# Kernel optimization log

Hardware: AMD Instinct MI355X
Metric: run time of the kernel (lower is better)

The kernel has to match this reference:

```python
import jax, jax.numpy as jnp
import numpy as np
from jax import lax

D_MODEL = 768
D_STATE = 16
D_CONV = 4
EXPAND = 1
D_INNER = D_MODEL * EXPAND  # 768
BATCH, SEQ = 8, 4096


def setup_inputs() -> dict:
    key = jax.random.key(0)
    ks = jax.random.split(key, 8)
    s = 0.02
    x = jax.random.normal(ks[0], (BATCH, SEQ, D_MODEL), jnp.float32)
    W_in = jax.random.normal(ks[1], (D_MODEL, 2 * D_INNER), jnp.float32) * s
    conv_w = jax.random.normal(ks[2], (D_INNER, 1, D_CONV), jnp.float32) * s  # depthwise (O, I/groups=1, K)
    W_x = jax.random.normal(ks[3], (D_INNER, D_STATE + D_MODEL), jnp.float32) * s
    A_log = jax.random.normal(ks[4], (D_MODEL, D_STATE), jnp.float32)
    Dp = jnp.ones((D_MODEL,), jnp.float32)
    W_out = jax.random.normal(ks[5], (D_INNER, D_MODEL), jnp.float32) * s
    gamma = jnp.ones((D_MODEL,), jnp.float32)
    beta = jnp.zeros((D_MODEL,), jnp.float32)
    return {"x": x, "W_in": W_in, "conv_w": conv_w, "W_x": W_x,
            "A_log": A_log, "Dp": Dp, "W_out": W_out, "gamma": gamma, "beta": beta}


def _layernorm(x, gamma, beta, eps=1e-5):
    mu = x.mean(-1, keepdims=True)
    var = ((x - mu) ** 2).mean(-1, keepdims=True)
    return (x - mu) * lax.rsqrt(var + eps) * gamma + beta


def reference(x, W_in, conv_w, W_x, A_log, Dp, W_out, gamma, beta):
    residual = x
    xn = _layernorm(x, gamma, beta)
    xz = xn @ W_in                                  # (b, l, 2*d_inner)
    x1, z = jnp.split(xz, 2, axis=-1)               # each (b, l, d_inner)
    # depthwise causal conv1d (left pad d_conv-1, truncate to L == causal)
    xc = jnp.transpose(x1, (0, 2, 1))               # (b, c, l)
    xc = lax.conv_general_dilated(
        xc, conv_w, window_strides=(1,), padding=[(D_CONV - 1, 0)],
        dimension_numbers=("NCH", "OIH", "NCH"), feature_group_count=D_INNER)
    x1 = jnp.transpose(xc, (0, 2, 1))               # (b, l, d_inner)
    ssm = x1 @ W_x                                  # (b, l, d_state + d_model)
    Bm = ssm[..., :D_STATE]                         # (b, l, d_state)
    Cm = ssm[..., D_STATE:]                         # (b, l, d_model)
    A = -jnp.exp(A_log)                             # (d_model, d_state)
    # pseudo-SSM mixing (valid-einsum interpretation of the source)
    h = jnp.einsum('bln,nd->bld', x1, A) + Bm * x1.sum(-1, keepdims=True)  # (b, l, d_state)
    y = Cm * h.sum(-1, keepdims=True) + Dp * x1     # (b, l, d_inner)
    y = y * jax.nn.silu(z)
    return y @ W_out + residual
```

## Files before the change

kernel.cpp:

```cpp
#include <hip/hip_runtime.h>

typedef __bf16 bf16_t;
typedef __bf16 bf16x8 __attribute__((ext_vector_type(8)));
typedef __bf16 bf16x4 __attribute__((ext_vector_type(4)));
typedef float f32x4 __attribute__((ext_vector_type(4)));

#define DM 768
#define SEQ_LEN 4096
#define TOKENS 32768

__device__ __forceinline__ void load16_to_lds(const void* g, void* l) {
  __builtin_amdgcn_global_load_lds(
      (const __attribute__((address_space(1))) unsigned int*)g,
      (__attribute__((address_space(3))) unsigned int*)l, 16, 0, 0);
}

__global__ __launch_bounds__(256)
void cast_transpose_kernel(const float* __restrict__ W, bf16_t* __restrict__ WT,
                           int K, int N, int stride, int off) {
  long idx = (long)blockIdx.x * 256 + threadIdx.x;
  if (idx >= (long)K * N) return;
  int n = (int)(idx / K);
  int k = (int)(idx % K);
  WT[idx] = (bf16_t)W[(long)k * stride + off + n];
}

__global__ __launch_bounds__(256)
void ab_kernel(const float* __restrict__ Wx, const float* __restrict__ A_log,
               float* __restrict__ a_vec, float* __restrict__ b_vec) {
  int k = blockIdx.x * 256 + threadIdx.x;
  if (k >= DM) return;
  float a = 0.f, b = 0.f;
#pragma unroll
  for (int d = 0; d < 16; d++) {
    a -= __expf(A_log[k * 16 + d]);
    b += Wx[(long)k * 784 + d];
  }
  a_vec[k] = a;
  b_vec[k] = b;
}

__global__ __launch_bounds__(256)
void ln_kernel(const float* __restrict__ x, const float* __restrict__ gamma,
               const float* __restrict__ beta, bf16_t* __restrict__ xn) {
  const int tok = blockIdx.x * 4 + (threadIdx.x >> 6);
  const int lane = threadIdx.x & 63;
  const float4* xr = (const float4*)(x + (long)tok * DM);
  float4 v0 = xr[lane], v1 = xr[lane + 64], v2 = xr[lane + 128];
  float s = v0.x + v0.y + v0.z + v0.w + v1.x + v1.y + v1.z + v1.w +
            v2.x + v2.y + v2.z + v2.w;
  float ss = v0.x * v0.x + v0.y * v0.y + v0.z * v0.z + v0.w * v0.w +
             v1.x * v1.x + v1.y * v1.y + v1.z * v1.z + v1.w * v1.w +
             v2.x * v2.x + v2.y * v2.y + v2.z * v2.z + v2.w * v2.w;
  for (int o = 1; o < 64; o <<= 1) { s += __shfl_xor(s, o); ss += __shfl_xor(ss, o); }
  float mu = s * (1.0f / DM);
  float var = ss * (1.0f / DM) - mu * mu;
  float inv = rsqrtf(var + 1e-5f);
  const float4* g4 = (const float4*)gamma;
  const float4* b4 = (const float4*)beta;
  bf16_t* xo = xn + (long)tok * DM;
#pragma unroll
  for (int i = 0; i < 3; i++) {
    float4 v = (i == 0) ? v0 : (i == 1) ? v1 : v2;
    float4 g = g4[lane + 64 * i], b = b4[lane + 64 * i];
    bf16x4 o;
    o[0] = (bf16_t)((v.x - mu) * inv * g.x + b.x);
    o[1] = (bf16_t)((v.y - mu) * inv * g.y + b.y);
    o[2] = (bf16_t)((v.z - mu) * inv * g.z + b.z);
    o[3] = (bf16_t)((v.w - mu) * inv * g.w + b.w);
    *(bf16x4*)(xo + lane * 4 + i * 256) = o;
  }
}

__global__ __launch_bounds__(256)
void conv_kernel(const bf16_t* __restrict__ xz, const float* __restrict__ conv_w,
                 const float* __restrict__ a_vec, const float* __restrict__ b_vec,
                 bf16_t* __restrict__ x1, float* __restrict__ hs) {
  const int tok = blockIdx.x * 4 + (threadIdx.x >> 6);
  const int lane = threadIdx.x & 63;
  const int l = tok & (SEQ_LEN - 1);
  const bf16_t* base = xz + (long)tok * 1536;
  const float4* w4 = (const float4*)conv_w;
  float s = 0.f, sa = 0.f, sb = 0.f;

  {
    const int c0 = lane * 8;
    bf16x8 cur = *(const bf16x8*)(base + c0);
    bf16x8 p1 = {}, p2 = {}, p3 = {};
    if (l >= 1) p1 = *(const bf16x8*)(base + c0 - 1536);
    if (l >= 2) p2 = *(const bf16x8*)(base + c0 - 2 * 1536);
    if (l >= 3) p3 = *(const bf16x8*)(base + c0 - 3 * 1536);
    bf16x8 o;
#pragma unroll
    for (int j = 0; j < 8; j++) {
      float4 w = w4[c0 + j];
      float acc = w.w * (float)cur[j] + w.z * (float)p1[j] +
                  w.y * (float)p2[j] + w.x * (float)p3[j];
      bf16_t xb = (bf16_t)acc;
      o[j] = xb;
      float xv = (float)xb;
      s += xv; sa += xv * a_vec[c0 + j]; sb += xv * b_vec[c0 + j];
    }
    *(bf16x8*)(x1 + (long)tok * DM + c0) = o;
  }
  {
    const int c0 = 512 + lane * 4;
    bf16x4 cur = *(const bf16x4*)(base + c0);
    bf16x4 p1 = {}, p2 = {}, p3 = {};
    if (l >= 1) p1 = *(const bf16x4*)(base + c0 - 1536);
    if (l >= 2) p2 = *(const bf16x4*)(base + c0 - 2 * 1536);
    if (l >= 3) p3 = *(const bf16x4*)(base + c0 - 3 * 1536);
    bf16x4 o;
#pragma unroll
    for (int j = 0; j < 4; j++) {
      float4 w = w4[c0 + j];
      float acc = w.w * (float)cur[j] + w.z * (float)p1[j] +
                  w.y * (float)p2[j] + w.x * (float)p3[j];
      bf16_t xb = (bf16_t)acc;
      o[j] = xb;
      float xv = (float)xb;
      s += xv; sa += xv * a_vec[c0 + j]; sb += xv * b_vec[c0 + j];
    }
    *(bf16x4*)(x1 + (long)tok * DM + c0) = o;
  }
  for (int o = 1; o < 64; o <<= 1) {
    s += __shfl_xor(s, o); sa += __shfl_xor(sa, o); sb += __shfl_xor(sb, o);
  }
  if (lane == 0) hs[tok] = sa + s * sb;
}

template <int OUT_MODE>
__global__ __launch_bounds__(512, 2)
void gemm256_kernel(const bf16_t* __restrict__ A, const bf16_t* __restrict__ BT,
                    void* __restrict__ outp, const float* __restrict__ res,
                    const bf16_t* __restrict__ x1, const bf16_t* __restrict__ xz,
                    const float* __restrict__ hs, const float* __restrict__ Dp,
                    int M, int N, int K) {
  __shared__ __align__(16) bf16_t As[2][256 * 64];
  __shared__ __align__(16) bf16_t Bs[2][256 * 64];

  const int nby = N >> 8;
  const int nwg = (M >> 8) * nby;
  const int cpx = nwg >> 3;
  const int wg = blockIdx.x;
  const int swz = (wg & 7) * cpx + (wg >> 3);
  const int bx = swz / nby;
  const int by = swz - bx * nby;
  const int m0 = bx << 8;
  const int n0 = by << 8;

  const int t = threadIdx.x;
  const int lane = t & 63;
  const int wave = t >> 6;
  const int wm = (wave >> 2) * 128;
  const int wn = (wave & 3) * 64;
  const int l15 = lane & 15;
  const int quad = lane >> 4;

  const int sx0 = (((0 * 4) + quad) ^ (lane & 7)) * 8;
  const int sx1 = (((1 * 4) + quad) ^ (lane & 7)) * 8;

  const int srow = lane >> 3;
  const int scol = (((lane & 7) ^ ((lane >> 3) & 7))) * 8;

  f32x4 acc[8][4] = {};
  bf16x8 a[4][2], b0[2][2], b1[2][2];

  const bf16_t* Abase = A + (long)m0 * K + scol;
  const bf16_t* Bbase = BT + (long)n0 * K + scol;

#define STAGE_A(buf, kt) do {                                               \
    const long kk_ = (long)(kt) * 64;                                       \
    _Pragma("unroll")                                                       \
    for (int h_ = 0; h_ < 2; h_++) {                                        \
      _Pragma("unroll")                                                     \
      for (int j_ = 0; j_ < 2; j_++) {                                      \
        const int rowl_ = h_ * 128 + wave * 16 + j_ * 8;                    \
        load16_to_lds(Abase + (long)(rowl_ + srow) * K + kk_,               \
                      &As[buf][rowl_ * 64]);                                \
      } } } while (0)

#define STAGE_B(buf, kt) do {                                               \
    const long kk_ = (long)(kt) * 64;                                       \
    _Pragma("unroll")                                                       \
    for (int h_ = 0; h_ < 2; h_++) {                                        \
      _Pragma("unroll")                                                     \
      for (int j_ = 0; j_ < 2; j_++) {                                      \
        const int rowl_ = h_ * 128 + wave * 16 + j_ * 8;                    \
        load16_to_lds(Bbase + (long)(rowl_ + srow) * K + kk_,               \
                      &Bs[buf][rowl_ * 64]);                                \
      } } } while (0)

#define READ_A(qm, buf) do {                                                \
    _Pragma("unroll")                                                       \
    for (int mi_ = 0; mi_ < 4; mi_++) {                                     \
      const bf16_t* p_ = &As[buf][(wm + (qm) * 64 + mi_ * 16 + l15) * 64];  \
      a[mi_][0] = *(const bf16x8*)(p_ + sx0);                               \
      a[mi_][1] = *(const bf16x8*)(p_ + sx1);                               \
    } } while (0)

#define READ_B(dst, qn, buf) do {                                           \
    _Pragma("unroll")                                                       \
    for (int ni_ = 0; ni_ < 2; ni_++) {                                     \
      const bf16_t* p_ = &Bs[buf][(wn + (qn) * 32 + ni_ * 16 + l15) * 64];  \
      dst[ni_][0] = *(const bf16x8*)(p_ + sx0);                             \
      dst[ni_][1] = *(const bf16x8*)(p_ + sx1);                             \
    } } while (0)

#define MFMA16(qm, qn, breg) do {                                           \
    __builtin_amdgcn_s_setprio(1);                                          \
    _Pragma("unroll")                                                       \
    for (int mi_ = 0; mi_ < 4; mi_++) {                                     \
      _Pragma("unroll")                                                     \
      for (int ni_ = 0; ni_ < 2; ni_++) {                                   \
        acc[(qm) * 4 + mi_][(qn) * 2 + ni_] =                               \
            __builtin_amdgcn_mfma_f32_16x16x32_bf16(                        \
                a[mi_][0], breg[ni_][0],                                    \
                acc[(qm) * 4 + mi_][(qn) * 2 + ni_], 0, 0, 0);              \
        acc[(qm) * 4 + mi_][(qn) * 2 + ni_] =                               \
            __builtin_amdgcn_mfma_f32_16x16x32_bf16(                        \
                a[mi_][1], breg[ni_][1],                                    \
                acc[(qm) * 4 + mi_][(qn) * 2 + ni_], 0, 0, 0);              \
      } }                                                                   \
    __builtin_amdgcn_s_setprio(0);                                          \
  } while (0)

#define BAR() do { asm volatile("" ::: "memory");                           \
    __builtin_amdgcn_s_barrier();                                           \
    asm volatile("" ::: "memory"); } while (0)

  const int NT = K >> 6;
  const int NI = NT >> 1;

  STAGE_A(0, 0);
  STAGE_B(0, 0);
  STAGE_A(1, 1);
  asm volatile("s_waitcnt vmcnt(4)" ::: "memory");
  BAR();

  for (int it = 0; it < NI; ++it) {
    const int t1k = 2 * it + 1;
    const int t2k = 2 * it + 2;
    const int t3k = 2 * it + 3;
    STAGE_B(1, t1k);
    READ_A(0, 0);
    READ_B(b0, 0, 0);
    BAR();
    MFMA16(0, 0, b0);
    READ_B(b1, 1, 0);
    BAR();
    MFMA16(0, 1, b1);
    READ_A(1, 0);
    BAR();
    MFMA16(1, 1, b1);
    if (t2k < NT) STAGE_A(0, t2k);
    MFMA16(1, 0, b0);
    if (t2k < NT) { asm volatile("s_waitcnt vmcnt(4)" ::: "memory"); }
    else          { asm volatile("s_waitcnt vmcnt(0)" ::: "memory"); }
    BAR();
    if (t2k < NT) STAGE_B(0, t2k);
    READ_A(0, 1);
    READ_B(b0, 0, 1);
    BAR();
    MFMA16(0, 0, b0);
    READ_B(b1, 1, 1);
    BAR();
    MFMA16(0, 1, b1);
    READ_A(1, 1);
    BAR();
    MFMA16(1, 1, b1);
    if (t3k < NT) STAGE_A(1, t3k);
    MFMA16(1, 0, b0);
    if (t3k < NT) { asm volatile("s_waitcnt vmcnt(4)" ::: "memory"); }
    else          { asm volatile("s_waitcnt vmcnt(0)" ::: "memory"); }
    BAR();
  }

#pragma unroll
  for (int mi = 0; mi < 8; mi++) {
#pragma unroll
    for (int r = 0; r < 4; r++) {
      const int row = m0 + wm + mi * 16 + quad * 4 + r;
      float hsv = 0.f;
      if (OUT_MODE == 1) hsv = hs[row];
#pragma unroll
      for (int ni = 0; ni < 4; ni++) {
        const int col = n0 + wn + ni * 16 + l15;
        const long o = (long)row * N + col;
        float v = acc[mi][ni][r];
        if (OUT_MODE == 0) {
          ((bf16_t*)outp)[o] = (bf16_t)v;
        } else if (OUT_MODE == 1) {
          float xv = (float)x1[(long)row * DM + col];
          float zv = (float)xz[(long)row * 1536 + DM + col];
          float yv = v * hsv + Dp[col] * xv;
          yv *= zv / (1.f + __expf(-zv));
          ((bf16_t*)outp)[o] = (bf16_t)yv;
        } else {
          ((float*)outp)[o] = v + res[o];
        }
      }
    }
  }
#undef STAGE_A
#undef STAGE_B
#undef READ_A
#undef READ_B
#undef MFMA16
#undef BAR
}

extern "C" void kernel_launch(void* const* d_in, const int* in_sizes, int n_in,
                              void* d_out, int out_size, void* d_ws, size_t ws_size,
                              hipStream_t stream) {
  const float* x      = (const float*)d_in[0];
  const float* W_in   = (const float*)d_in[1];
  const float* conv_w = (const float*)d_in[2];
  const float* W_x    = (const float*)d_in[3];
  const float* A_log  = (const float*)d_in[4];
  const float* Dp     = (const float*)d_in[5];
  const float* W_out  = (const float*)d_in[6];
  const float* gamma  = (const float*)d_in[7];
  const float* beta   = (const float*)d_in[8];
  float* out = (float*)d_out;

  char* ws = (char*)d_ws;
  bf16_t* w_in_T  = (bf16_t*)(ws + 0);
  bf16_t* w_c_T   = (bf16_t*)(ws + 2359296);
  bf16_t* w_out_T = (bf16_t*)(ws + 3538944);
  float*  a_vec   = (float*)(ws + 4718592);
  float*  b_vec   = (float*)(ws + 4721664);
  float*  hs      = (float*)(ws + 4724736);
  bf16_t* xn      = (bf16_t*)(ws + 4855808);
  bf16_t* xz      = (bf16_t*)(ws + 55187456);
  bf16_t* x1      = (bf16_t*)(ws + 155850752);
  bf16_t* y       = xn;

  cast_transpose_kernel<<<dim3(1536 * 768 / 256), 256, 0, stream>>>(W_in, w_in_T, 768, 1536, 1536, 0);
  cast_transpose_kernel<<<dim3(768 * 768 / 256), 256, 0, stream>>>(W_x, w_c_T, 768, 768, 784, 16);
  cast_transpose_kernel<<<dim3(768 * 768 / 256), 256, 0, stream>>>(W_out, w_out_T, 768, 768, 768, 0);
  ab_kernel<<<dim3(3), 256, 0, stream>>>(W_x, A_log, a_vec, b_vec);

  ln_kernel<<<dim3(TOKENS / 4), 256, 0, stream>>>(x, gamma, beta, xn);

  gemm256_kernel<0><<<dim3((TOKENS / 256) * (1536 / 256)), 512, 0, stream>>>(
      xn, w_in_T, (void*)xz, nullptr, nullptr, nullptr, nullptr, nullptr,
      TOKENS, 1536, 768);

  conv_kernel<<<dim3(TOKENS / 4), 256, 0, stream>>>(xz, conv_w, a_vec, b_vec, x1, hs);

  gemm256_kernel<1><<<dim3((TOKENS / 256) * (768 / 256)), 512, 0, stream>>>(
      x1, w_c_T, (void*)y, nullptr, x1, xz, hs, Dp,
      TOKENS, 768, 768);

  gemm256_kernel<2><<<dim3((TOKENS / 256) * (768 / 256)), 512, 0, stream>>>(
      y, w_out_T, (void*)out, x, nullptr, nullptr, nullptr, nullptr,
      TOKENS, 768, 768);
}
```

Before: 511.3 us.

## Merge prep kernels into one launch and use 128x128 GEMM for N=768

Folds the three weight cast-transposes, the A/B vector reduction and the layernorm into a single prep kernel that dispatches work by block-id range, removing four launches. Adds a new 128x128-tile, 256-thread GEMM with a k-step of 32 and an XCD-aware block swizzle, and uses it for the two N=768 GEMMs instead of the 256x256 kernel. The goal is more workgroups for better CU occupancy on the smaller GEMMs, at the cost of a simpler, unpipelined single-buffered loop with two barriers per k-step.

```diff
diff --git a/kernel.cpp b/kernel.cpp
--- a/kernel.cpp
+++ b/kernel.cpp
@@ -16,59 +16,66 @@
 }
 
 __global__ __launch_bounds__(256)
-void cast_transpose_kernel(const float* __restrict__ W, bf16_t* __restrict__ WT,
-                           int K, int N, int stride, int off) {
-  long idx = (long)blockIdx.x * 256 + threadIdx.x;
-  if (idx >= (long)K * N) return;
-  int n = (int)(idx / K);
-  int k = (int)(idx % K);
-  WT[idx] = (bf16_t)W[(long)k * stride + off + n];
-}
-
-__global__ __launch_bounds__(256)
-void ab_kernel(const float* __restrict__ Wx, const float* __restrict__ A_log,
-               float* __restrict__ a_vec, float* __restrict__ b_vec) {
-  int k = blockIdx.x * 256 + threadIdx.x;
-  if (k >= DM) return;
-  float a = 0.f, b = 0.f;
-#pragma unroll
-  for (int d = 0; d < 16; d++) {
-    a -= __expf(A_log[k * 16 + d]);
-    b += Wx[(long)k * 784 + d];
-  }
-  a_vec[k] = a;
-  b_vec[k] = b;
-}
-
-__global__ __launch_bounds__(256)
-void ln_kernel(const float* __restrict__ x, const float* __restrict__ gamma,
-               const float* __restrict__ beta, bf16_t* __restrict__ xn) {
-  const int tok = blockIdx.x * 4 + (threadIdx.x >> 6);
-  const int lane = threadIdx.x & 63;
-  const float4* xr = (const float4*)(x + (long)tok * DM);
-  float4 v0 = xr[lane], v1 = xr[lane + 64], v2 = xr[lane + 128];
-  float s = v0.x + v0.y + v0.z + v0.w + v1.x + v1.y + v1.z + v1.w +
-            v2.x + v2.y + v2.z + v2.w;
-  float ss = v0.x * v0.x + v0.y * v0.y + v0.z * v0.z + v0.w * v0.w +
-             v1.x * v1.x + v1.y * v1.y + v1.z * v1.z + v1.w * v1.w +
-             v2.x * v2.x + v2.y * v2.y + v2.z * v2.z + v2.w * v2.w;
-  for (int o = 1; o < 64; o <<= 1) { s += __shfl_xor(s, o); ss += __shfl_xor(ss, o); }
-  float mu = s * (1.0f / DM);
-  float var = ss * (1.0f / DM) - mu * mu;
-  float inv = rsqrtf(var + 1e-5f);
-  const float4* g4 = (const float4*)gamma;
-  const float4* b4 = (const float4*)beta;
-  bf16_t* xo = xn + (long)tok * DM;
-#pragma unroll
-  for (int i = 0; i < 3; i++) {
-    float4 v = (i == 0) ? v0 : (i == 1) ? v1 : v2;
-    float4 g = g4[lane + 64 * i], b = b4[lane + 64 * i];
-    bf16x4 o;
-    o[0] = (bf16_t)((v.x - mu) * inv * g.x + b.x);
-    o[1] = (bf16_t)((v.y - mu) * inv * g.y + b.y);
-    o[2] = (bf16_t)((v.z - mu) * inv * g.z + b.z);
-    o[3] = (bf16_t)((v.w - mu) * inv * g.w + b.w);
-    *(bf16x4*)(xo + lane * 4 + i * 256) = o;
+void prep_kernel(const float* __restrict__ W_in, const float* __restrict__ W_x,
+                 const float* __restrict__ W_out, const float* __restrict__ A_log,
+                 const float* __restrict__ x, const float* __restrict__ gamma,
+                 const float* __restrict__ beta,
+                 bf16_t* __restrict__ w_in_T, bf16_t* __restrict__ w_c_T,
+                 bf16_t* __restrict__ w_out_T, float* __restrict__ a_vec,
+                 float* __restrict__ b_vec, bf16_t* __restrict__ xn) {
+  const int bid = blockIdx.x;
+  if (bid < 4608) {
+    int idx = bid * 256 + threadIdx.x;
+    int n = idx / 768, k = idx - n * 768;
+    w_in_T[idx] = (bf16_t)W_in[k * 1536 + n];
+  } else if (bid < 6912) {
+    int idx = (bid - 4608) * 256 + threadIdx.x;
+    int n = idx / 768, k = idx - n * 768;
+    w_c_T[idx] = (bf16_t)W_x[k * 784 + 16 + n];
+  } else if (bid < 9216) {
+    int idx = (bid - 6912) * 256 + threadIdx.x;
+    int n = idx / 768, k = idx - n * 768;
+    w_out_T[idx] = (bf16_t)W_out[k * 768 + n];
+  } else if (bid < 9219) {
+    int k = (bid - 9216) * 256 + threadIdx.x;
+    if (k < DM) {
+      float a = 0.f, b = 0.f;
+#pragma unroll
+      for (int d = 0; d < 16; d++) {
+        a -= __expf(A_log[k * 16 + d]);
+        b += W_x[(long)k * 784 + d];
+      }
+      a_vec[k] = a;
+      b_vec[k] = b;
+    }
+  } else {
+    const int tok = (bid - 9219) * 4 + (threadIdx.x >> 6);
+    const int lane = threadIdx.x & 63;
+    const float4* xr = (const float4*)(x + (long)tok * DM);
+    float4 v0 = xr[lane], v1 = xr[lane + 64], v2 = xr[lane + 128];
+    float s = v0.x + v0.y + v0.z + v0.w + v1.x + v1.y + v1.z + v1.w +
+              v2.x + v2.y + v2.z + v2.w;
+    float ss = v0.x * v0.x + v0.y * v0.y + v0.z * v0.z + v0.w * v0.w +
+               v1.x * v1.x + v1.y * v1.y + v1.z * v1.z + v1.w * v1.w +
+               v2.x * v2.x + v2.y * v2.y + v2.z * v2.z + v2.w * v2.w;
+    for (int o = 1; o < 64; o <<= 1) { s += __shfl_xor(s, o); ss += __shfl_xor(ss, o); }
+    float mu = s * (1.0f / DM);
+    float var = ss * (1.0f / DM) - mu * mu;
+    float inv = rsqrtf(var + 1e-5f);
+    const float4* g4 = (const float4*)gamma;
+    const float4* b4 = (const float4*)beta;
+    bf16_t* xo = xn + (long)tok * DM;
+#pragma unroll
+    for (int i = 0; i < 3; i++) {
+      float4 v = (i == 0) ? v0 : (i == 1) ? v1 : v2;
+      float4 g = g4[lane + 64 * i], b = b4[lane + 64 * i];
+      bf16x4 o;
+      o[0] = (bf16_t)((v.x - mu) * inv * g.x + b.x);
+      o[1] = (bf16_t)((v.y - mu) * inv * g.y + b.y);
+      o[2] = (bf16_t)((v.z - mu) * inv * g.z + b.z);
+      o[3] = (bf16_t)((v.w - mu) * inv * g.w + b.w);
+      *(bf16x4*)(xo + lane * 4 + i * 256) = o;
+    }
   }
 }
 
@@ -310,6 +317,103 @@
 #undef BAR
 }
 
+template <int OUT_MODE>
+__global__ __launch_bounds__(256, 3)
+void gemm128_kernel(const bf16_t* __restrict__ A, const bf16_t* __restrict__ BT,
+                    void* __restrict__ outp, const float* __restrict__ res,
+                    const bf16_t* __restrict__ x1, const bf16_t* __restrict__ xz,
+                    const float* __restrict__ hs, const float* __restrict__ Dp,
+                    int M, int N, int K) {
+  __shared__ __align__(16) bf16_t As[128 * 32];
+  __shared__ __align__(16) bf16_t Bs[128 * 32];
+
+  const int nby = N >> 7;
+  const int nwg = (M >> 7) * nby;
+  const int cpx = nwg >> 3;
+  const int wg = blockIdx.x;
+  const int swz = (wg & 7) * cpx + (wg >> 3);
+  const int bx = swz / nby;
+  const int by = swz - bx * nby;
+  const int m0 = bx << 7;
+  const int n0 = by << 7;
+
+  const int t = threadIdx.x;
+  const int lane = t & 63;
+  const int wave = t >> 6;
+  const int wm = (wave >> 1) * 64;
+  const int wn = (wave & 1) * 64;
+  const int l15 = lane & 15;
+  const int quad = lane >> 4;
+
+  f32x4 acc[4][4] = {};
+
+  const int sr = lane >> 2;
+  const int sc = (lane & 3) * 8;
+  const bf16_t* Ag[2];
+  bf16_t* lA[2];
+#pragma unroll
+  for (int i = 0; i < 2; i++) {
+    int ch = wave * 2 + i;
+    Ag[i] = A + (long)(m0 + ch * 16 + sr) * K + sc;
+    lA[i] = As + ch * 512 + lane * 8;
+  }
+  const bf16_t* Bg[2];
+  bf16_t* lB[2];
+#pragma unroll
+  for (int i = 0; i < 2; i++) {
+    int ch = wave * 2 + i;
+    Bg[i] = BT + (long)(n0 + ch * 16 + sr) * K + sc;
+    lB[i] = Bs + ch * 512 + lane * 8;
+  }
+
+  for (int k0 = 0; k0 < K; k0 += 32) {
+#pragma unroll
+    for (int i = 0; i < 2; i++) load16_to_lds(Ag[i] + k0, lA[i]);
+#pragma unroll
+    for (int i = 0; i < 2; i++) load16_to_lds(Bg[i] + k0, lB[i]);
+    __syncthreads();
+    bf16x8 bfrag[4];
+#pragma unroll
+    for (int ni = 0; ni < 4; ni++)
+      bfrag[ni] = *(const bf16x8*)&Bs[(wn + ni * 16 + l15) * 32 + quad * 8];
+#pragma unroll
+    for (int mi = 0; mi < 4; mi++) {
+      bf16x8 afrag = *(const bf16x8*)&As[(wm + mi * 16 + l15) * 32 + quad * 8];
+#pragma unroll
+      for (int ni = 0; ni < 4; ni++)
+        acc[mi][ni] = __builtin_amdgcn_mfma_f32_16x16x32_bf16(afrag, bfrag[ni], acc[mi][ni], 0, 0, 0);
+    }
+    __syncthreads();
+  }
+
+#pragma unroll
+  for (int mi = 0; mi < 4; mi++) {
+#pragma unroll
+    for (int r = 0; r < 4; r++) {
+      const int row = m0 + wm + mi * 16 + quad * 4 + r;
+      float hsv = 0.f;
+      if (OUT_MODE == 1) hsv = hs[row];
+#pragma unroll
+      for (int ni = 0; ni < 4; ni++) {
+        const int col = n0 + wn + ni * 16 + l15;
+        const long o = (long)row * N + col;
+        float v = acc[mi][ni][r];
+        if (OUT_MODE == 0) {
+          ((bf16_t*)outp)[o] = (bf16_t)v;
+        } else if (OUT_MODE == 1) {
+          float xv = (float)x1[(long)row * DM + col];
+          float zv = (float)xz[(long)row * 1536 + DM + col];
+          float yv = v * hsv + Dp[col] * xv;
+          yv *= zv / (1.f + __expf(-zv));
+          ((bf16_t*)outp)[o] = (bf16_t)yv;
+        } else {
+          ((float*)outp)[o] = v + res[o];
+        }
+      }
+    }
+  }
+}
+
 extern "C" void kernel_launch(void* const* d_in, const int* in_sizes, int n_in,
                               void* d_out, int out_size, void* d_ws, size_t ws_size,
                               hipStream_t stream) {
@@ -336,12 +440,9 @@
   bf16_t* x1      = (bf16_t*)(ws + 155850752);
   bf16_t* y       = xn;
 
-  cast_transpose_kernel<<<dim3(1536 * 768 / 256), 256, 0, stream>>>(W_in, w_in_T, 768, 1536, 1536, 0);
-  cast_transpose_kernel<<<dim3(768 * 768 / 256), 256, 0, stream>>>(W_x, w_c_T, 768, 768, 784, 16);
-  cast_transpose_kernel<<<dim3(768 * 768 / 256), 256, 0, stream>>>(W_out, w_out_T, 768, 768, 768, 0);
-  ab_kernel<<<dim3(3), 256, 0, stream>>>(W_x, A_log, a_vec, b_vec);
-
-  ln_kernel<<<dim3(TOKENS / 4), 256, 0, stream>>>(x, gamma, beta, xn);
+  prep_kernel<<<dim3(17411), 256, 0, stream>>>(
+      W_in, W_x, W_out, A_log, x, gamma, beta,
+      w_in_T, w_c_T, w_out_T, a_vec, b_vec, xn);
 
   gemm256_kernel<0><<<dim3((TOKENS / 256) * (1536 / 256)), 512, 0, stream>>>(
       xn, w_in_T, (void*)xz, nullptr, nullptr, nullptr, nullptr, nullptr,
@@ -349,11 +450,11 @@
 
   conv_kernel<<<dim3(TOKENS / 4), 256, 0, stream>>>(xz, conv_w, a_vec, b_vec, x1, hs);
 
-  gemm256_kernel<1><<<dim3((TOKENS / 256) * (768 / 256)), 512, 0, stream>>>(
+  gemm128_kernel<1><<<dim3((TOKENS / 128) * (768 / 128)), 256, 0, stream>>>(
       x1, w_c_T, (void*)y, nullptr, x1, xz, hs, Dp,
       TOKENS, 768, 768);
 
-  gemm256_kernel<2><<<dim3((TOKENS / 256) * (768 / 256)), 512, 0, stream>>>(
+  gemm128_kernel<2><<<dim3((TOKENS / 128) * (768 / 128)), 256, 0, stream>>>(
       y, w_out_T, (void*)out, x, nullptr, nullptr, nullptr, nullptr,
       TOKENS, 768, 768);
 }
```

Result: faster. 476.1 us (-6.9%).
